# Kernel tuning notes

Hardware: AMD Instinct MI355X
Metric: run time of the kernel (lower is better)

Reference implementation:

```python
import jax, jax.numpy as jnp
import numpy as np

N = 8192          # num nodes
D = 512           # num_hidden
P = 512           # num_proj_hidden
TAU = 0.5
EPS = 1e-12       # F.normalize eps


def setup_inputs() -> dict:
    key = jax.random.key(0)
    k1, k2, k3, k4, k5, k6 = jax.random.split(key, 6)
    s1 = 1.0 / np.sqrt(D)  # torch Linear init bound
    s2 = 1.0 / np.sqrt(P)
    return {
        "z1": jax.random.normal(k1, (N, D), jnp.float32),
        "z2": jax.random.normal(k2, (N, D), jnp.float32),
        "index": jnp.arange(N, dtype=jnp.int32),  # all-unique -> unique() identity path
        "fc1_w": jax.random.uniform(k3, (D, P), jnp.float32, -s1, s1),
        "fc1_b": jax.random.uniform(k4, (P,), jnp.float32, -s1, s1),
        "fc2_w": jax.random.uniform(k5, (P, D), jnp.float32, -s2, s2),
        "fc2_b": jax.random.uniform(k6, (D,), jnp.float32, -s2, s2),
    }


def _projection(z, fc1_w, fc1_b, fc2_w, fc2_b):
    h = jax.nn.elu(z @ fc1_w + fc1_b)
    return h @ fc2_w + fc2_b


def _normalize(x):
    n = jnp.linalg.norm(x, axis=1, keepdims=True)
    return x / jnp.maximum(n, EPS)


def _semi_loss(a, b):
    an = _normalize(a)
    bn = _normalize(b)
    refl = jnp.exp((an @ an.T) / TAU)      # [N, N]
    btw = jnp.exp((an @ bn.T) / TAU)       # [N, N]
    denom = refl.sum(axis=1) + btw.sum(axis=1) - jnp.diagonal(refl)
    return -jnp.log(jnp.diagonal(btw) / denom)  # [N]


def reference(z1, z2, index, fc1_w, fc1_b, fc2_w, fc2_b):
    h1 = _projection(z1, fc1_w, fc1_b, fc2_w, fc2_b)
    h2 = _projection(z2, fc1_w, fc1_b, fc2_w, fc2_b)
    # index is all-unique (arange) -> unique() returns (h1, h2) unchanged
    l1 = _semi_loss(h1, h2)
    l2 = _semi_loss(h2, h1)
    return ((l1 + l2) * 0.5).mean()
```

## Files before the change

### kernel.cpp

```cpp
#include <hip/hip_runtime.h>
#include <hip/hip_bf16.h>

typedef __attribute__((ext_vector_type(8))) short short8;
typedef __attribute__((ext_vector_type(4))) short short4v;
typedef __attribute__((ext_vector_type(4))) float floatx4;
typedef __attribute__((ext_vector_type(2))) long longx2;
typedef __attribute__((ext_vector_type(2))) unsigned int uintx2;

#define NND 8192
#define DHID 512
#define TAU_INV 2.0f
#define CEXP 2.885390081777927f
#define E2 7.389056098930650f

__device__ inline unsigned short f2bf(float f) {
    union { float f; unsigned u; } v; v.f = f;
    unsigned r = v.u + 0x7FFFu + ((v.u >> 16) & 1u);
    return (unsigned short)(r >> 16);
}
__device__ inline float bf2f(short s) {
    union { unsigned u; float f; } v; v.u = ((unsigned)(unsigned short)s) << 16;
    return v.f;
}

__device__ inline void gload_lds16(const void* g, void* l) {
    __builtin_amdgcn_global_load_lds(
        (const __attribute__((address_space(1))) unsigned int*)g,
        (__attribute__((address_space(3))) unsigned int*)l,
        16, 0, 0);
}

__device__ inline short8 cvt8(floatx4 a, floatx4 b) {
    short8 o;
    o[0] = (short)f2bf(a[0]); o[1] = (short)f2bf(a[1]);
    o[2] = (short)f2bf(a[2]); o[3] = (short)f2bf(a[3]);
    o[4] = (short)f2bf(b[0]); o[5] = (short)f2bf(b[1]);
    o[6] = (short)f2bf(b[2]); o[7] = (short)f2bf(b[3]);
    return o;
}

__global__ void transpose_cast2(const float* __restrict__ a, const float* __restrict__ b,
                                short* __restrict__ oa, short* __restrict__ ob) {
    int idx = blockIdx.x * 256 + threadIdx.x;
    const float* in = (idx < 262144) ? a : b;
    short* out = (idx < 262144) ? oa : ob;
    idx &= 262143;
    int n = idx >> 9, k = idx & 511;
    out[(n << 9) + k] = (short)f2bf(in[(k << 9) + n]);
}

#define BK 32

template<int MODE>
__global__ __launch_bounds__(256, 2)
void gemm_nt(const float* __restrict__ Az1, const float* __restrict__ Az2,
             const short* __restrict__ Abf, const short* __restrict__ B,
             const float* __restrict__ bias, short* __restrict__ outBf)
{
    __shared__ short As[128 * BK];
    __shared__ short Bs[128 * BK];

    const int tid  = threadIdx.x;
    const int m0 = blockIdx.x * 128;
    const int n0 = blockIdx.y * 128;
    const int wave = tid >> 6;
    const int lane = tid & 63;
    const int wr   = wave >> 1;
    const int wc   = wave & 1;
    const int lrow = lane & 15;
    const int lk   = lane >> 4;
    const int swq  = (lk ^ ((lrow >> 1) & 3)) * 8;

    const int r0 = tid >> 2;
    const int qq = tid & 3;
    const int q  = qq ^ ((r0 >> 1) & 3);

    const float* Asrc = (MODE == 0)
        ? ((m0 < NND) ? Az1 + (size_t)m0 * 512 : Az2 + (size_t)(m0 - NND) * 512)
        : nullptr;

    floatx4 acc[4][4];
    floatx4 zero4 = {0.f, 0.f, 0.f, 0.f};
#pragma unroll
    for (int m = 0; m < 4; ++m)
#pragma unroll
        for (int n = 0; n < 4; ++n) acc[m][n] = zero4;

    for (int kt = 0; kt < 512 / BK; ++kt) {
        const int k0 = kt * BK;
        floatx4 a00, a01, a10, a11;
        if (MODE == 0) {
            const float* p0 = Asrc + (size_t)r0 * 512 + k0 + q * 8;
            const float* p1 = Asrc + (size_t)(r0 + 64) * 512 + k0 + q * 8;
            a00 = *(const floatx4*)p0;  a01 = *(const floatx4*)(p0 + 4);
            a10 = *(const floatx4*)p1;  a11 = *(const floatx4*)(p1 + 4);
        }
        __syncthreads();
        if (MODE == 0) {
            *(short8*)&As[r0 * 32 + qq * 8]        = cvt8(a00, a01);
            *(short8*)&As[(r0 + 64) * 32 + qq * 8] = cvt8(a10, a11);
            gload_lds16(B + (size_t)(n0 + r0) * 512 + k0 + q * 8,        &Bs[r0 * 32 + qq * 8]);
            gload_lds16(B + (size_t)(n0 + 64 + r0) * 512 + k0 + q * 8,   &Bs[(r0 + 64) * 32 + qq * 8]);
        } else {
#pragma unroll
            for (int i = 0; i < 2; ++i) {
                const int r = i * 64 + r0;
                gload_lds16(Abf + (size_t)(m0 + r) * 512 + k0 + q * 8, &As[r * 32 + qq * 8]);
                gload_lds16(B   + (size_t)(n0 + r) * 512 + k0 + q * 8, &Bs[r * 32 + qq * 8]);
            }
        }
        __syncthreads();
        short8 fa[4], fb[4];
#pragma unroll
        for (int m = 0; m < 4; ++m)
            fa[m] = *(const short8*)(&As[(wr * 64 + m * 16 + lrow) * 32 + swq]);
#pragma unroll
        for (int n = 0; n < 4; ++n)
            fb[n] = *(const short8*)(&Bs[(wc * 64 + n * 16 + lrow) * 32 + swq]);
#pragma unroll
        for (int m = 0; m < 4; ++m)
#pragma unroll
            for (int n = 0; n < 4; ++n)
                acc[m][n] = __builtin_amdgcn_mfma_f32_16x16x32_bf16(fa[m], fb[n], acc[m][n], 0, 0, 0);
    }

#pragma unroll
    for (int m = 0; m < 4; ++m) {
#pragma unroll
        for (int n = 0; n < 4; ++n) {
            const int gj = n0 + wc * 64 + n * 16 + lrow;
            const float bj = bias[gj];
#pragma unroll
            for (int r = 0; r < 4; ++r) {
                const int gi = m0 + wr * 64 + m * 16 + lk * 4 + r;
                float v = acc[m][n][r] + bj;
                if (MODE == 0) v = v > 0.f ? v : expm1f(v);
                outBf[(size_t)gi * 512 + gj] = (short)f2bf(v);
            }
        }
    }
}

__global__ __launch_bounds__(256, 3)
void gemm_gram(const unsigned char* __restrict__ Q, float* __restrict__ gpart)
{
    __shared__ unsigned char As[3][128 * 64];
    __shared__ unsigned char Bs[3][128 * 64];

    const int tid = threadIdx.x;
    const int wg = blockIdx.x;
    int bj = (int)((sqrtf(8.0f * (float)wg + 1.0f) - 1.0f) * 0.5f);
    if (bj < 0) bj = 0;
    if (bj > 127) bj = 127;
    while (bj > 0 && bj * (bj + 1) / 2 > wg) --bj;
    while ((bj + 1) * (bj + 2) / 2 <= wg) ++bj;
    const int bi = wg - bj * (bj + 1) / 2;
    const int m0 = bi * 128, n0 = bj * 128;

    const int wave = tid >> 6;
    const int lane = tid & 63;
    const int wr   = wave >> 1;
    const int wc   = wave & 1;
    const int lrow = lane & 15;
    const int lk   = lane >> 4;

    const int sr = tid >> 2;
    const int qL = tid & 3;
    const int qG = qL ^ ((sr >> 1) & 3);

#define STAGE_G(buf, k0) do { \
    gload_lds16(Q + (size_t)(m0 + sr) * 512 + (k0) + qG * 16,      &As[buf][ sr       * 64 + qL * 16]); \
    gload_lds16(Q + (size_t)(m0 + 64 + sr) * 512 + (k0) + qG * 16, &As[buf][(sr + 64) * 64 + qL * 16]); \
    gload_lds16(Q + (size_t)(n0 + sr) * 512 + (k0) + qG * 16,      &Bs[buf][ sr       * 64 + qL * 16]); \
    gload_lds16(Q + (size_t)(n0 + 64 + sr) * 512 + (k0) + qG * 16, &Bs[buf][(sr + 64) * 64 + qL * 16]); \
} while (0)

    floatx4 acc[4][4];
    floatx4 zero4 = {0.f, 0.f, 0.f, 0.f};
#pragma unroll
    for (int m = 0; m < 4; ++m)
#pragma unroll
        for (int n = 0; n < 4; ++n) acc[m][n] = zero4;

    STAGE_G(0, 0);
    STAGE_G(1, 64);
    asm volatile("s_waitcnt vmcnt(4)" ::: "memory");
    __builtin_amdgcn_s_barrier();

#pragma unroll
    for (int kt = 0; kt < 8; ++kt) {
        const int cur = kt % 3;
        if (kt + 2 < 8) STAGE_G((kt + 2) % 3, (kt + 2) * 64);
        longx2 fb[4];
#pragma unroll
        for (int n = 0; n < 4; ++n) {
            const int row = wc * 64 + n * 16 + lrow;
            fb[n] = *(const longx2*)&Bs[cur][(row << 6) + ((lk ^ ((row >> 1) & 3)) << 4)];
        }
#pragma unroll
        for (int m = 0; m < 4; ++m) {
            const int row = wr * 64 + m * 16 + lrow;
            const longx2 fa = *(const longx2*)&As[cur][(row << 6) + ((lk ^ ((row >> 1) & 3)) << 4)];
#pragma unroll
            for (int n = 0; n < 4; ++n) {
                acc[m][n] = __builtin_amdgcn_mfma_f32_16x16x32_fp8_fp8(fa[0], fb[n][0], acc[m][n], 0, 0, 0);
                acc[m][n] = __builtin_amdgcn_mfma_f32_16x16x32_fp8_fp8(fa[1], fb[n][1], acc[m][n], 0, 0, 0);
            }
        }
        if (kt < 6) asm volatile("s_waitcnt vmcnt(4)" ::: "memory");
        else        asm volatile("s_waitcnt vmcnt(0)" ::: "memory");
        __builtin_amdgcn_s_barrier();
    }
#undef STAGE_G

    float* lred = (float*)&As[0][0];

    float colpart[4] = {0.f, 0.f, 0.f, 0.f};
#pragma unroll
    for (int m = 0; m < 4; ++m) {
        float rowpart[4] = {0.f, 0.f, 0.f, 0.f};
#pragma unroll
        for (int n = 0; n < 4; ++n) {
#pragma unroll
            for (int r = 0; r < 4; ++r) {
                float v = exp2f(acc[m][n][r] * CEXP);
                rowpart[r] += v;
                colpart[n] += v;
            }
        }
#pragma unroll
        for (int r = 0; r < 4; ++r) {
            float t = rowpart[r];
            t += __shfl_xor(t, 1);
            t += __shfl_xor(t, 2);
            t += __shfl_xor(t, 4);
            t += __shfl_xor(t, 8);
            if (lrow == 0) lred[wc * 128 + wr * 64 + m * 16 + lk * 4 + r] = t;
        }
    }
#pragma unroll
    for (int n = 0; n < 4; ++n) {
        float t = colpart[n];
        t += __shfl_xor(t, 16);
        t += __shfl_xor(t, 32);
        if (lk == 0) lred[256 + wr * 128 + wc * 64 + n * 16 + lrow] = t;
    }
    __syncthreads();

    if (tid < 128) {
        gpart[(size_t)bj * (2 * NND) + m0 + tid] = lred[tid] + lred[128 + tid];
    } else if (m0 != n0) {
        const int c = tid - 128;
        gpart[(size_t)bi * (2 * NND) + n0 + c] = lred[256 + c] + lred[384 + c];
    }
}

__global__ void reduce_partials(const float* __restrict__ gpart, float* __restrict__ rsG) {
    const int i = blockIdx.x * 256 + threadIdx.x;
    float s = 0.f;
#pragma unroll 8
    for (int sl = 0; sl < 128; ++sl)
        s += gpart[(size_t)sl * (2 * NND) + i];
    rsG[i] = s;
}

__global__ void normalize_diag(const short* __restrict__ o, unsigned char* __restrict__ anq,
                               float* __restrict__ d12) {
    const int row = blockIdx.x;
    const int t = threadIdx.x;
    short4v va = ((const short4v*)(o + ((size_t)row << 9)))[t];
    short4v vb = ((const short4v*)(o + ((size_t)(row + NND) << 9)))[t];
    const float a0 = bf2f(va[0]), a1 = bf2f(va[1]), a2 = bf2f(va[2]), a3 = bf2f(va[3]);
    const float b0 = bf2f(vb[0]), b1 = bf2f(vb[1]), b2 = bf2f(vb[2]), b3 = bf2f(vb[3]);
    float ssa = a0 * a0 + a1 * a1 + a2 * a2 + a3 * a3;
    float ssb = b0 * b0 + b1 * b1 + b2 * b2 + b3 * b3;
    float sd  = a0 * b0 + a1 * b1 + a2 * b2 + a3 * b3;
    for (int m = 1; m < 64; m <<= 1) {
        ssa += __shfl_xor(ssa, m);
        ssb += __shfl_xor(ssb, m);
        sd  += __shfl_xor(sd, m);
    }
    __shared__ float part[6];
    if ((t & 63) == 0) {
        const int w = (t >> 6) * 3;
        part[w] = ssa; part[w + 1] = ssb; part[w + 2] = sd;
    }
    __syncthreads();
    const float sca = 1.f / fmaxf(sqrtf(part[0] + part[3]), 1e-12f);
    const float scb = 1.f / fmaxf(sqrtf(part[1] + part[4]), 1e-12f);
    if (t == 0) d12[row] = (part[2] + part[5]) * sca * scb;

    const int k = t * 4;
    const int bb = k >> 6, kk = k & 63;
    const int off = (bb << 6) + (((kk & 31) >> 3) << 4) + ((kk >> 5) << 3) + (kk & 7);
    int wa = __builtin_amdgcn_cvt_pk_fp8_f32(a0 * sca, a1 * sca, 0, false);
    wa = __builtin_amdgcn_cvt_pk_fp8_f32(a2 * sca, a3 * sca, wa, true);
    *(int*)(anq + (row << 9) + off) = wa;
    int wb = __builtin_amdgcn_cvt_pk_fp8_f32(b0 * scb, b1 * scb, 0, false);
    wb = __builtin_amdgcn_cvt_pk_fp8_f32(b2 * scb, b3 * scb, wb, true);
    *(int*)(anq + ((size_t)(row + NND) << 9) + off) = wb;
}

__global__ void final_reduce(const float* __restrict__ rsG,
                             const float* __restrict__ d12, float* __restrict__ out) {
    float s = 0.f;
    for (int i = threadIdx.x; i < NND; i += 256) {
        const float den1 = rsG[i] - E2;
        const float den2 = rsG[i + NND] - E2;
        s += 0.5f * (logf(den1) + logf(den2)) - d12[i] * TAU_INV;
    }
    for (int m = 1; m < 64; m <<= 1) s += __shfl_xor(s, m);
    __shared__ float part[4];
    const int lane = threadIdx.x & 63, w = threadIdx.x >> 6;
    if (lane == 0) part[w] = s;
    __syncthreads();
    if (threadIdx.x == 0) out[0] = (part[0] + part[1] + part[2] + part[3]) / (float)NND;
}

extern "C" void kernel_launch(void* const* d_in, const int* in_sizes, int n_in,
                              void* d_out, int out_size, void* d_ws, size_t ws_size,
                              hipStream_t stream) {
    const float* z1 = (const float*)d_in[0];
    const float* z2 = (const float*)d_in[1];
    const float* w1 = (const float*)d_in[3];
    const float* b1 = (const float*)d_in[4];
    const float* w2 = (const float*)d_in[5];
    const float* b2 = (const float*)d_in[6];
    float* out = (float*)d_out;

    char* p = (char*)d_ws;
    const size_t MATB = (size_t)2 * NND * DHID * 2;
    short* hb  = (short*)p;  p += MATB;
    short* obuf = (short*)p; p += MATB;
    unsigned char* anq = (unsigned char*)p; p += (size_t)2 * NND * DHID;
    float* gpart = (float*)p; p += (size_t)128 * 2 * NND * 4;
    short* w1t = (short*)p;  p += 512 * 512 * 2;
    short* w2t = (short*)p;  p += 512 * 512 * 2;
    float* rsG = (float*)p;  p += (size_t)2 * NND * 4;
    float* d12 = (float*)p;  p += NND * 4;
    if ((size_t)(p - (char*)d_ws) > ws_size) return;

    transpose_cast2<<<2048, 256, 0, stream>>>(w1, w2, w1t, w2t);
    gemm_nt<0><<<dim3(128, 4), 256, 0, stream>>>(z1, z2, nullptr, w1t, b1, hb);
    gemm_nt<1><<<dim3(128, 4), 256, 0, stream>>>(nullptr, nullptr, hb, w2t, b2, obuf);
    normalize_diag<<<NND, 128, 0, stream>>>(obuf, anq, d12);

    gemm_gram<<<8256, 256, 0, stream>>>(anq, gpart);
    reduce_partials<<<64, 256, 0, stream>>>(gpart, rsG);

    final_reduce<<<1, 256, 0, stream>>>(rsG, d12, out);
}
```

Measured before the change: 195.0 us.

## Enlarge gram GEMM tiles to 256x256 with 8 waves and phased staging

The triangular gram kernel moves from 128x128 tiles with 4 waves to 256x256 tiles with 8 waves per 512-thread block. Each wave now holds an 8x4 MFMA accumulator block, and each k-step is split into four phases that interleave one slice of the next-stage global-to-LDS loads with MFMA work, with s_setprio raised around the MFMAs. The aim is more arithmetic per byte loaded from memory and fewer blocks and partials, with reduce_partials now summing 64 slices. The cost is larger LDS use (96KB), one block per CU, more barriers per k-step, and more tile-level imbalance along the diagonal.

Result: slower. 253.2 us (+29.8%).

```diff
diff --git a/kernel.cpp b/kernel.cpp
--- a/kernel.cpp
+++ b/kernel.cpp
@@ -99,8 +99,8 @@
         if (MODE == 0) {
             *(short8*)&As[r0 * 32 + qq * 8]        = cvt8(a00, a01);
             *(short8*)&As[(r0 + 64) * 32 + qq * 8] = cvt8(a10, a11);
-            gload_lds16(B + (size_t)(n0 + r0) * 512 + k0 + q * 8,        &Bs[r0 * 32 + qq * 8]);
-            gload_lds16(B + (size_t)(n0 + 64 + r0) * 512 + k0 + q * 8,   &Bs[(r0 + 64) * 32 + qq * 8]);
+            gload_lds16(B + (size_t)(n0 + r0) * 512 + k0 + q * 8,      &Bs[r0 * 32 + qq * 8]);
+            gload_lds16(B + (size_t)(n0 + 64 + r0) * 512 + k0 + q * 8, &Bs[(r0 + 64) * 32 + qq * 8]);
         } else {
 #pragma unroll
             for (int i = 0; i < 2; ++i) {
@@ -141,26 +141,27 @@
     }
 }
 
-__global__ __launch_bounds__(256, 3)
+
+__global__ __launch_bounds__(512, 1)
 void gemm_gram(const unsigned char* __restrict__ Q, float* __restrict__ gpart)
 {
-    __shared__ unsigned char As[3][128 * 64];
-    __shared__ unsigned char Bs[3][128 * 64];
+    __shared__ unsigned char As[3][256 * 64];
+    __shared__ unsigned char Bs[3][256 * 64];
 
     const int tid = threadIdx.x;
     const int wg = blockIdx.x;
     int bj = (int)((sqrtf(8.0f * (float)wg + 1.0f) - 1.0f) * 0.5f);
     if (bj < 0) bj = 0;
-    if (bj > 127) bj = 127;
+    if (bj > 63) bj = 63;
     while (bj > 0 && bj * (bj + 1) / 2 > wg) --bj;
     while ((bj + 1) * (bj + 2) / 2 <= wg) ++bj;
     const int bi = wg - bj * (bj + 1) / 2;
-    const int m0 = bi * 128, n0 = bj * 128;
+    const int m0 = bi * 256, n0 = bj * 256;
 
     const int wave = tid >> 6;
     const int lane = tid & 63;
-    const int wr   = wave >> 1;
-    const int wc   = wave & 1;
+    const int wr   = wave >> 2;
+    const int wc   = wave & 3;
     const int lrow = lane & 15;
     const int lk   = lane >> 4;
 
@@ -169,16 +170,23 @@
     const int qG = qL ^ ((sr >> 1) & 3);
 
 #define STAGE_G(buf, k0) do { \
-    gload_lds16(Q + (size_t)(m0 + sr) * 512 + (k0) + qG * 16,      &As[buf][ sr       * 64 + qL * 16]); \
-    gload_lds16(Q + (size_t)(m0 + 64 + sr) * 512 + (k0) + qG * 16, &As[buf][(sr + 64) * 64 + qL * 16]); \
-    gload_lds16(Q + (size_t)(n0 + sr) * 512 + (k0) + qG * 16,      &Bs[buf][ sr       * 64 + qL * 16]); \
-    gload_lds16(Q + (size_t)(n0 + 64 + sr) * 512 + (k0) + qG * 16, &Bs[buf][(sr + 64) * 64 + qL * 16]); \
+    gload_lds16(Q + (size_t)(m0 + sr) * 512 + (k0) + qG * 16,       &As[buf][ sr        * 64 + qL * 16]); \
+    gload_lds16(Q + (size_t)(m0 + 128 + sr) * 512 + (k0) + qG * 16, &As[buf][(sr + 128) * 64 + qL * 16]); \
+    gload_lds16(Q + (size_t)(n0 + sr) * 512 + (k0) + qG * 16,       &Bs[buf][ sr        * 64 + qL * 16]); \
+    gload_lds16(Q + (size_t)(n0 + 128 + sr) * 512 + (k0) + qG * 16, &Bs[buf][(sr + 128) * 64 + qL * 16]); \
 } while (0)
 
-    floatx4 acc[4][4];
+#define STAGE_1(buf, k0, c) do { \
+    if ((c) == 0) gload_lds16(Q + (size_t)(m0 + sr) * 512 + (k0) + qG * 16,       &As[buf][ sr        * 64 + qL * 16]); \
+    if ((c) == 1) gload_lds16(Q + (size_t)(m0 + 128 + sr) * 512 + (k0) + qG * 16, &As[buf][(sr + 128) * 64 + qL * 16]); \
+    if ((c) == 2) gload_lds16(Q + (size_t)(n0 + sr) * 512 + (k0) + qG * 16,       &Bs[buf][ sr        * 64 + qL * 16]); \
+    if ((c) == 3) gload_lds16(Q + (size_t)(n0 + 128 + sr) * 512 + (k0) + qG * 16, &Bs[buf][(sr + 128) * 64 + qL * 16]); \
+} while (0)
+
+    floatx4 acc[8][4];
     floatx4 zero4 = {0.f, 0.f, 0.f, 0.f};
 #pragma unroll
-    for (int m = 0; m < 4; ++m)
+    for (int m = 0; m < 8; ++m)
 #pragma unroll
         for (int n = 0; n < 4; ++n) acc[m][n] = zero4;
 
@@ -190,34 +198,49 @@
 #pragma unroll
     for (int kt = 0; kt < 8; ++kt) {
         const int cur = kt % 3;
-        if (kt + 2 < 8) STAGE_G((kt + 2) % 3, (kt + 2) * 64);
-        longx2 fb[4];
-#pragma unroll
-        for (int n = 0; n < 4; ++n) {
-            const int row = wc * 64 + n * 16 + lrow;
-            fb[n] = *(const longx2*)&Bs[cur][(row << 6) + ((lk ^ ((row >> 1) & 3)) << 4)];
-        }
-#pragma unroll
-        for (int m = 0; m < 4; ++m) {
-            const int row = wr * 64 + m * 16 + lrow;
-            const longx2 fa = *(const longx2*)&As[cur][(row << 6) + ((lk ^ ((row >> 1) & 3)) << 4)];
-#pragma unroll
-            for (int n = 0; n < 4; ++n) {
-                acc[m][n] = __builtin_amdgcn_mfma_f32_16x16x32_fp8_fp8(fa[0], fb[n][0], acc[m][n], 0, 0, 0);
-                acc[m][n] = __builtin_amdgcn_mfma_f32_16x16x32_fp8_fp8(fa[1], fb[n][1], acc[m][n], 0, 0, 0);
-            }
-        }
-        if (kt < 6) asm volatile("s_waitcnt vmcnt(4)" ::: "memory");
-        else        asm volatile("s_waitcnt vmcnt(0)" ::: "memory");
-        __builtin_amdgcn_s_barrier();
+        const int nxt = (kt + 2) % 3;
+#pragma unroll
+        for (int ph = 0; ph < 4; ++ph) {
+            const int mh = ph >> 1, nh = ph & 1;
+            longx2 fa[4], fb[2];
+#pragma unroll
+            for (int n = 0; n < 2; ++n) {
+                const int row = wc * 64 + (nh * 2 + n) * 16 + lrow;
+                fb[n] = *(const longx2*)&Bs[cur][(row << 6) + ((lk ^ ((row >> 1) & 3)) << 4)];
+            }
+#pragma unroll
+            for (int m = 0; m < 4; ++m) {
+                const int row = wr * 128 + (mh * 4 + m) * 16 + lrow;
+                fa[m] = *(const longx2*)&As[cur][(row << 6) + ((lk ^ ((row >> 1) & 3)) << 4)];
+            }
+            if (kt + 2 < 8) STAGE_1(nxt, (kt + 2) * 64, ph);
+            __builtin_amdgcn_s_barrier();
+            __builtin_amdgcn_s_setprio(1);
+#pragma unroll
+            for (int m = 0; m < 4; ++m)
+#pragma unroll
+                for (int n = 0; n < 2; ++n) {
+                    acc[mh * 4 + m][nh * 2 + n] = __builtin_amdgcn_mfma_f32_16x16x32_fp8_fp8(
+                        fa[m][0], fb[n][0], acc[mh * 4 + m][nh * 2 + n], 0, 0, 0);
+                    acc[mh * 4 + m][nh * 2 + n] = __builtin_amdgcn_mfma_f32_16x16x32_fp8_fp8(
+                        fa[m][1], fb[n][1], acc[mh * 4 + m][nh * 2 + n], 0, 0, 0);
+                }
+            __builtin_amdgcn_s_setprio(0);
+            if (ph == 3) {
+                if (kt < 6) asm volatile("s_waitcnt vmcnt(4)" ::: "memory");
+                else        asm volatile("s_waitcnt vmcnt(0)" ::: "memory");
+            }
+            __builtin_amdgcn_s_barrier();
+        }
     }
 #undef STAGE_G
+#undef STAGE_1
 
     float* lred = (float*)&As[0][0];
 
     float colpart[4] = {0.f, 0.f, 0.f, 0.f};
 #pragma unroll
-    for (int m = 0; m < 4; ++m) {
+    for (int m = 0; m < 8; ++m) {
         float rowpart[4] = {0.f, 0.f, 0.f, 0.f};
 #pragma unroll
         for (int n = 0; n < 4; ++n) {
@@ -235,7 +258,7 @@
             t += __shfl_xor(t, 2);
             t += __shfl_xor(t, 4);
             t += __shfl_xor(t, 8);
-            if (lrow == 0) lred[wc * 128 + wr * 64 + m * 16 + lk * 4 + r] = t;
+            if (lrow == 0) lred[wc * 256 + wr * 128 + m * 16 + lk * 4 + r] = t;
         }
     }
 #pragma unroll
@@ -243,15 +266,16 @@
         float t = colpart[n];
         t += __shfl_xor(t, 16);
         t += __shfl_xor(t, 32);
-        if (lk == 0) lred[256 + wr * 128 + wc * 64 + n * 16 + lrow] = t;
+        if (lk == 0) lred[1024 + wr * 256 + wc * 64 + n * 16 + lrow] = t;
     }
     __syncthreads();
 
-    if (tid < 128) {
-        gpart[(size_t)bj * (2 * NND) + m0 + tid] = lred[tid] + lred[128 + tid];
+    if (tid < 256) {
+        gpart[(size_t)bj * (2 * NND) + m0 + tid] =
+            lred[tid] + lred[256 + tid] + lred[512 + tid] + lred[768 + tid];
     } else if (m0 != n0) {
-        const int c = tid - 128;
-        gpart[(size_t)bi * (2 * NND) + n0 + c] = lred[256 + c] + lred[384 + c];
+        const int c = tid - 256;
+        gpart[(size_t)bi * (2 * NND) + n0 + c] = lred[1024 + c] + lred[1280 + c];
     }
 }
 
@@ -259,7 +283,7 @@
     const int i = blockIdx.x * 256 + threadIdx.x;
     float s = 0.f;
 #pragma unroll 8
-    for (int sl = 0; sl < 128; ++sl)
+    for (int sl = 0; sl < 64; ++sl)
         s += gpart[(size_t)sl * (2 * NND) + i];
     rsG[i] = s;
 }
@@ -333,7 +357,7 @@
     short* hb  = (short*)p;  p += MATB;
     short* obuf = (short*)p; p += MATB;
     unsigned char* anq = (unsigned char*)p; p += (size_t)2 * NND * DHID;
-    float* gpart = (float*)p; p += (size_t)128 * 2 * NND * 4;
+    float* gpart = (float*)p; p += (size_t)64 * 2 * NND * 4;
     short* w1t = (short*)p;  p += 512 * 512 * 2;
     short* w2t = (short*)p;  p += 512 * 512 * 2;
     float* rsG = (float*)p;  p += (size_t)2 * NND * 4;
@@ -345,7 +369,7 @@
     gemm_nt<1><<<dim3(128, 4), 256, 0, stream>>>(nullptr, nullptr, hb, w2t, b2, obuf);
     normalize_diag<<<NND, 128, 0, stream>>>(obuf, anq, d12);
 
-    gemm_gram<<<8256, 256, 0, stream>>>(anq, gpart);
+    gemm_gram<<<2080, 512, 0, stream>>>(anq, gpart);
     reduce_partials<<<64, 256, 0, stream>>>(gpart, rsG);
 
     final_reduce<<<1, 256, 0, stream>>>(rsG, d12, out);
```
